# Kernel optimization log

Hardware: AMD Instinct MI355X
Metric: run time of the kernel (lower is better)

## Reference

```python
import jax, jax.numpy as jnp
import numpy as np

D_MODEL = 2048
N_HEADS = 16
HEAD_DIM = D_MODEL // N_HEADS


def setup_inputs() -> dict:
    key = jax.random.key(0)
    k_x, k_wqkv, k_bqkv, k_wo, k_bo = jax.random.split(key, 5)
    s = 1.0 / np.sqrt(D_MODEL)
    return {
        "x": jax.random.normal(k_x, (2, 2048, D_MODEL), dtype=jnp.float32),
        "w_qkv": jax.random.uniform(k_wqkv, (D_MODEL, 3 * D_MODEL), jnp.float32, -s, s),
        "b_qkv": jax.random.uniform(k_bqkv, (3 * D_MODEL,), jnp.float32, -s, s),
        "w_out": jax.random.uniform(k_wo, (D_MODEL, D_MODEL), jnp.float32, -s, s),
        "b_out": jax.random.uniform(k_bo, (D_MODEL,), jnp.float32, -s, s),
    }


def reference(x, w_qkv, b_qkv, w_out, b_out):
    b, l, d = x.shape
    h, e = N_HEADS, HEAD_DIM
    qkv = x @ w_qkv + b_qkv                       # [b, l, 3d]
    q, k, v = jnp.split(qkv, 3, axis=-1)
    # split heads: [b, l, d] -> [b, l, h, e]
    q = q.reshape(b, l, h, e)
    k = k.reshape(b, l, h, e)
    v = v.reshape(b, l, h, e)
    scale = 1.0 / np.sqrt(e).astype(np.float32)
    scores = jnp.einsum("bqhe,bkhe->bhqk", q, k) * scale  # [b, h, l, l]
    attn = jax.nn.softmax(scores, axis=-1)                 # non-causal (module hardcodes is_causal=False)
    out = jnp.einsum("bhqk,bkhe->bqhe", attn, v)           # [b, l, h, e]
    out = out.reshape(b, l, d)                             # merge heads
    return out @ w_out + b_out
```

## Files before the change

### kernel.cpp

```cpp
#include <hip/hip_runtime.h>

typedef __attribute__((ext_vector_type(8))) short bf16x8;
typedef __attribute__((ext_vector_type(4))) float f32x4;
typedef __attribute__((ext_vector_type(16))) float f32x16;
typedef __attribute__((ext_vector_type(4))) int int4v;
typedef __attribute__((ext_vector_type(4))) unsigned short us4;

#define LOG2E 1.4426950408889634f

__device__ __forceinline__ unsigned short f2b(float f){
  unsigned u = __builtin_bit_cast(unsigned, f);
  u = (u + 0x7fffu + ((u >> 16) & 1u)) >> 16;
  return (unsigned short)u;
}
__device__ __forceinline__ unsigned short f2bf(float f){
  unsigned u = __builtin_bit_cast(unsigned, f);
  return (unsigned short)((u + 0x8000u) >> 16);
}

__device__ __forceinline__ f32x4 mfma16(bf16x8 a, bf16x8 b, f32x4 c){
  return __builtin_amdgcn_mfma_f32_16x16x32_bf16(a, b, c, 0, 0, 0);
}
__device__ __forceinline__ f32x16 mfma32(bf16x8 a, bf16x8 b, f32x16 c){
  return __builtin_amdgcn_mfma_f32_32x32x16_bf16(a, b, c, 0, 0, 0);
}

typedef const __attribute__((address_space(1))) void* gas_t;
typedef __attribute__((address_space(3))) void* las_t;
__device__ __forceinline__ void glds16(const void* g, void* l){
  __builtin_amdgcn_global_load_lds((gas_t)g, (las_t)l, 16, 0, 0);
}

__global__ __launch_bounds__(256) void cast_bf16_kernel(const float4* __restrict__ in,
                                                        us4* __restrict__ out, int n4){
  int i = blockIdx.x * 256 + threadIdx.x;
  int stride = gridDim.x * 256;
  for (; i < n4; i += stride){
    float4 v = in[i];
    us4 o; o.x = f2b(v.x); o.y = f2b(v.y); o.z = f2b(v.z); o.w = f2b(v.w);
    out[i] = o;
  }
}

__global__ __launch_bounds__(256) void transpose2_kernel(const float* __restrict__ in0,
                                                         unsigned short* __restrict__ out0,
                                                         const float* __restrict__ in1,
                                                         unsigned short* __restrict__ out1){
  __shared__ float tile[64][65];
  const int tid = threadIdx.x;
  const bool first = blockIdx.x < 96;
  const float* in = first ? in0 : in1;
  unsigned short* out = first ? out0 : out1;
  const int C = first ? 6144 : 2048;
  const int R = 2048;
  const int bx = first ? blockIdx.x : blockIdx.x - 96;
  const int c0 = bx * 64, r0 = blockIdx.y * 64;
#pragma unroll
  for (int p = 0; p < 4; p++){
    int idx = p * 1024 + tid * 4;
    int rr = idx >> 6, cc = idx & 63;
    float4 v = *(const float4*)(in + (size_t)(r0 + rr) * C + (c0 + cc));
    tile[rr][cc+0] = v.x; tile[rr][cc+1] = v.y; tile[rr][cc+2] = v.z; tile[rr][cc+3] = v.w;
  }
  __syncthreads();
#pragma unroll
  for (int p = 0; p < 4; p++){
    int idx = p * 1024 + tid * 4;
    int crow = idx >> 6, rcol = idx & 63;
    us4 o;
    o.x = f2b(tile[rcol+0][crow]); o.y = f2b(tile[rcol+1][crow]);
    o.z = f2b(tile[rcol+2][crow]); o.w = f2b(tile[rcol+3][crow]);
    *(us4*)(out + (size_t)(c0 + crow) * R + (r0 + rcol)) = o;
  }
}

template<int MODE>
__global__ __launch_bounds__(256, 2) void gemm_kernel(
    const unsigned short* __restrict__ A,
    const unsigned short* __restrict__ BT,
    const float* __restrict__ bias,
    unsigned short* __restrict__ qb,
    unsigned short* __restrict__ kb,
    unsigned short* __restrict__ vtb,
    float* __restrict__ outp,
    int cpx, int nbm)
{
  constexpr int K = 2048;
  constexpr int NT = K / 64;
  __shared__ short lA[2][128 * 64];
  __shared__ short lB[2][128 * 64];
  const int tid = threadIdx.x, lane = tid & 63, wid = tid >> 6;
  const int l16 = lane & 15, lhi = lane >> 4;
  const int wr = wid >> 1, wc = wid & 1;

  const int id = blockIdx.x;
  const int logical = (id & 7) * cpx + (id >> 3);
  const int bm = logical % nbm, bn = logical / nbm;

  const char* Abase = (const char*)(A + (size_t)bm * 128 * K);
  const char* Bbase = (const char*)(BT + (size_t)bn * 128 * K);

  const char* agp[4]; const char* bgp[4];
  int dst[4];
#pragma unroll
  for (int i = 0; i < 4; i++){
    int c = wid * 4 + i;
    int row = c * 8 + (lane >> 3);
    int col = ((lane & 7) * 16) ^ ((lane >> 3) << 4);
    agp[i] = Abase + (size_t)row * (K * 2) + col;
    bgp[i] = Bbase + (size_t)row * (K * 2) + col;
    dst[i] = c * 1024;
  }

  auto stage = [&](int kt, int buf){
    char* bA = (char*)lA[buf]; char* bB = (char*)lB[buf];
#pragma unroll
    for (int i = 0; i < 4; i++){
      glds16(agp[i] + kt * 128, bA + dst[i]);
      glds16(bgp[i] + kt * 128, bB + dst[i]);
    }
  };

  f32x4 acc[4][4];
  f32x4 z = {0.f, 0.f, 0.f, 0.f};
#pragma unroll
  for (int i = 0; i < 4; i++)
#pragma unroll
    for (int j = 0; j < 4; j++) acc[i][j] = z;

  stage(0, 0);
  __syncthreads();
  int cur = 0;
  for (int kt = 0; kt < NT; ++kt){
    if (kt + 1 < NT) stage(kt + 1, cur ^ 1);
#pragma unroll
    for (int kk = 0; kk < 2; kk++){
      bf16x8 af[4], bfr[4];
#pragma unroll
      for (int mf = 0; mf < 4; mf++){
        int row = wr * 64 + mf * 16 + l16;
        int byte = (row * 128 + kk * 64 + lhi * 16) ^ ((row & 7) << 4);
        af[mf] = *(const bf16x8*)((const char*)lA[cur] + byte);
      }
#pragma unroll
      for (int nf = 0; nf < 4; nf++){
        int row = wc * 64 + nf * 16 + l16;
        int byte = (row * 128 + kk * 64 + lhi * 16) ^ ((row & 7) << 4);
        bfr[nf] = *(const bf16x8*)((const char*)lB[cur] + byte);
      }
      __builtin_amdgcn_s_setprio(1);
#pragma unroll
      for (int mf = 0; mf < 4; mf++)
#pragma unroll
        for (int nf = 0; nf < 4; nf++)
          acc[mf][nf] = mfma16(af[mf], bfr[nf], acc[mf][nf]);
      __builtin_amdgcn_s_setprio(0);
    }
    __syncthreads();
    cur ^= 1;
  }

  const int row0 = bm * 128 + wr * 64;
  const int col0 = bn * 128 + wc * 64;
  if (MODE == 0){
#pragma unroll
    for (int nf = 0; nf < 4; nf++){
      int colb = col0 + nf * 16;
      float bv = bias[colb + l16];
      int which = colb >> 11;
      int h = (colb >> 7) & 15;
      int e = (colb & 127) + l16;
#pragma unroll
      for (int mf = 0; mf < 4; mf++){
#pragma unroll
        for (int r = 0; r < 4; r++){
          int row = row0 + mf * 16 + lhi * 4 + r;
          int b = row >> 11, t = row & 2047;
          float v = acc[mf][nf][r] + bv;
          size_t bh = (size_t)(b * 16 + h);
          if (which == 0)      qb[(bh * 2048 + t) * 128 + e] = f2b(v * 0.08838834764831845f);
          else if (which == 1) kb[(bh * 2048 + t) * 128 + e] = f2b(v);
          else                 vtb[(bh * 128 + e) * 2048 + t] = f2b(v);
        }
      }
    }
  } else {
#pragma unroll
    for (int nf = 0; nf < 4; nf++){
      int col = col0 + nf * 16 + l16;
      float bv = bias[col];
#pragma unroll
      for (int mf = 0; mf < 4; mf++){
#pragma unroll
        for (int r = 0; r < 4; r++){
          int row = row0 + mf * 16 + lhi * 4 + r;
          outp[(size_t)row * 2048 + col] = acc[mf][nf][r] + bv;
        }
      }
    }
  }
}

__global__ __launch_bounds__(256, 2) void attn_kernel(
    const unsigned short* __restrict__ q_buf,
    const unsigned short* __restrict__ k_buf,
    const unsigned short* __restrict__ vt_buf,
    unsigned short* __restrict__ attn_out)
{
  constexpr int L = 2048, NT = L / 64;
  __shared__ short lK[2][64 * 128];
  __shared__ short lVT[2][128 * 64];
  const int tid = threadIdx.x, lane = tid & 63, wid = tid >> 6;
  const int l31 = lane & 31, lhi2 = lane >> 5;

  const int d = blockIdx.y * 16 + blockIdx.x;
  const int bh = (d & 7) + 8 * ((d >> 3) & 3);
  const int qi = d >> 5;
  const int qbase = qi * 128;

  const unsigned short* qp = q_buf + (size_t)bh * L * 128;
  const char* kp2 = (const char*)(k_buf + (size_t)bh * L * 128);
  const char* vp2 = (const char*)(vt_buf + (size_t)bh * 128 * L);

  bf16x8 qf[8];
  {
    const unsigned short* qr = qp + (size_t)(qbase + wid * 32 + l31) * 128 + lhi2 * 8;
#pragma unroll
    for (int kk = 0; kk < 8; kk++)
      qf[kk] = *(const bf16x8*)(qr + kk * 16);
  }

  const char* kgp[4]; const char* vgp[4];
  int kdst[4], vdst[4];
#pragma unroll
  for (int i = 0; i < 4; i++){
    int c = wid * 4 + i;
    { int row = c * 4 + (lane >> 4);
      int col = ((lane & 15) * 16) ^ ((row & 7) << 4);
      kgp[i] = kp2 + row * 256 + col;
      kdst[i] = c * 1024; }
    { int e = c * 8 + (lane >> 3);
      int col = ((lane & 7) * 16) ^ ((e & 7) << 4);
      vgp[i] = vp2 + (size_t)e * 4096 + col;
      vdst[i] = c * 1024; }
  }

  auto stage = [&](int kt, int buf){
    char* bK = (char*)lK[buf]; char* bV = (char*)lVT[buf];
#pragma unroll
    for (int i = 0; i < 4; i++){
      glds16(kgp[i] + kt * 16384, bK + kdst[i]);
      glds16(vgp[i] + (size_t)kt * 128, bV + vdst[i]);
    }
  };

  f32x16 oacc[4];
#pragma unroll
  for (int nf = 0; nf < 4; nf++)
#pragma unroll
    for (int j = 0; j < 16; j++) oacc[nf][j] = 0.f;
  float m = -1e30f, ml2 = 0.f, lsum = 0.f;

  stage(0, 0);
  __syncthreads();
  int cur = 0;
  for (int kt = 0; kt < NT; ++kt){
    if (kt + 1 < NT) stage(kt + 1, cur ^ 1);
    const char* cK = (const char*)lK[cur];
    const char* cV = (const char*)lVT[cur];

    f32x16 sf[2];
#pragma unroll
    for (int mf = 0; mf < 2; mf++)
#pragma unroll
      for (int j = 0; j < 16; j++) sf[mf][j] = 0.f;
    __builtin_amdgcn_s_setprio(1);
#pragma unroll
    for (int kk = 0; kk < 8; kk++){
#pragma unroll
      for (int mf = 0; mf < 2; mf++){
        int byte = ((l31 * 256 + kk * 32 + lhi2 * 16) ^ ((l31 & 7) << 4)) + mf * 8192;
        bf16x8 kf = *(const bf16x8*)(cK + byte);
        sf[mf] = mfma32(kf, qf[kk], sf[mf]);
      }
    }
    __builtin_amdgcn_s_setprio(0);

    float tm = sf[0][0];
#pragma unroll
    for (int mf = 0; mf < 2; mf++)
#pragma unroll
      for (int j = 0; j < 16; j++) tm = fmaxf(tm, sf[mf][j]);
    tm = fmaxf(tm, __shfl_xor(tm, 32, 64));

    if (!__all(tm <= m + 8.0f)){
      float mn = fmaxf(m, tm);
      float alpha = __builtin_exp2f((m - mn) * LOG2E);
      m = mn; ml2 = mn * LOG2E;
      lsum *= alpha;
#pragma unroll
      for (int reg = 0; reg < 16; reg++){
        int row = (reg & 3) + 8 * (reg >> 2) + 4 * lhi2;
        float ar = __shfl(alpha, row | (lane & 32), 64);
#pragma unroll
        for (int nf = 0; nf < 4; nf++) oacc[nf][reg] *= ar;
      }
    }

    float pex[2][16];
    float rs = 0.f;
#pragma unroll
    for (int mf = 0; mf < 2; mf++)
#pragma unroll
      for (int j = 0; j < 16; j++){
        float p = __builtin_exp2f(__builtin_fmaf(sf[mf][j], LOG2E, -ml2));
        pex[mf][j] = p; rs += p;
      }
    rs += __shfl_xor(rs, 32, 64);
    lsum += rs;

    unsigned W[2][4][2];
#pragma unroll
    for (int mf = 0; mf < 2; mf++)
#pragma unroll
      for (int g = 0; g < 4; g++)
#pragma unroll
        for (int h = 0; h < 2; h++)
          W[mf][g][h] = (unsigned)f2bf(pex[mf][g * 4 + 2 * h]) |
                        ((unsigned)f2bf(pex[mf][g * 4 + 2 * h + 1]) << 16);

    __builtin_amdgcn_s_setprio(1);
#pragma unroll
    for (int kk2 = 0; kk2 < 4; kk2++){
      const int mfp = kk2 >> 1, gA = 2 * (kk2 & 1), gB = gA + 1;
      unsigned A0 = W[mfp][gA][0], A1 = W[mfp][gA][1];
      unsigned B0 = W[mfp][gB][0], B1 = W[mfp][gB][1];
      unsigned own0 = lhi2 ? B0 : A0, own1 = lhi2 ? B1 : A1;
      unsigned snd0 = lhi2 ? A0 : B0, snd1 = lhi2 ? A1 : B1;
      unsigned rcv0 = (unsigned)__shfl_xor((int)snd0, 32, 64);
      unsigned rcv1 = (unsigned)__shfl_xor((int)snd1, 32, 64);
      int4v pw;
      pw.x = (int)(lhi2 ? rcv0 : own0);
      pw.y = (int)(lhi2 ? rcv1 : own1);
      pw.z = (int)(lhi2 ? own0 : rcv0);
      pw.w = (int)(lhi2 ? own1 : rcv1);
      bf16x8 pa = __builtin_bit_cast(bf16x8, pw);
#pragma unroll
      for (int nf = 0; nf < 4; nf++){
        int byte = ((l31 * 128 + kk2 * 32 + lhi2 * 16) ^ ((l31 & 7) << 4)) + nf * 4096;
        bf16x8 vb = *(const bf16x8*)(cV + byte);
        oacc[nf] = mfma32(pa, vb, oacc[nf]);
      }
    }
    __builtin_amdgcn_s_setprio(0);

    __syncthreads();
    cur ^= 1;
  }

  const int b = bh >> 4, h = bh & 15;
  float rl = 1.0f / lsum;
#pragma unroll
  for (int reg = 0; reg < 16; reg++){
    int row = (reg & 3) + 8 * (reg >> 2) + 4 * lhi2;
    float rr = __shfl(rl, row | (lane & 32), 64);
    size_t base = ((size_t)(b * L + qbase + wid * 32 + row)) * 2048 + h * 128 + l31;
#pragma unroll
    for (int nf = 0; nf < 4; nf++)
      attn_out[base + nf * 32] = f2b(oacc[nf][reg] * rr);
  }
}

extern "C" void kernel_launch(void* const* d_in, const int* in_sizes, int n_in,
                              void* d_out, int out_size, void* d_ws, size_t ws_size,
                              hipStream_t stream) {
  const float* x     = (const float*)d_in[0];
  const float* w_qkv = (const float*)d_in[1];
  const float* b_qkv = (const float*)d_in[2];
  const float* w_out = (const float*)d_in[3];
  const float* b_out = (const float*)d_in[4];
  float* out = (float*)d_out;

  unsigned short* ws = (unsigned short*)d_ws;
  unsigned short* xb    = ws;
  unsigned short* wqkvT = xb    + (size_t)4096 * 2048;
  unsigned short* woutT = wqkvT + (size_t)6144 * 2048;
  unsigned short* qb    = woutT + (size_t)2048 * 2048;
  unsigned short* kb    = qb    + (size_t)2 * 16 * 2048 * 128;
  unsigned short* vtb   = kb    + (size_t)2 * 16 * 2048 * 128;
  unsigned short* attnb = vtb   + (size_t)2 * 16 * 2048 * 128;

  cast_bf16_kernel<<<2048, 256, 0, stream>>>((const float4*)x, (us4*)xb, (4096 * 2048) / 4);
  transpose2_kernel<<<dim3(128, 32), 256, 0, stream>>>(w_qkv, wqkvT, w_out, woutT);
  gemm_kernel<0><<<1536, 256, 0, stream>>>(xb, wqkvT, b_qkv, qb, kb, vtb, nullptr, 192, 32);
  attn_kernel<<<dim3(16, 32), 256, 0, stream>>>(qb, kb, vtb, attnb);
  gemm_kernel<1><<<512, 256, 0, stream>>>(attnb, woutT, b_out, nullptr, nullptr, nullptr, out, 64, 32);
}
```

Baseline: 303.4 us.

## Use 512-thread GEMM blocks with 8 waves and drop the block swizzle

The GEMM block grows from 4 to 8 waves, so each wave computes a 64x32 sub-tile instead of 64x64 and global-to-LDS staging is spread over twice as many threads. Fewer accumulators per wave and launch bounds of 4 aim for more resident waves to hide latency. The XCD-aware block index remapping is replaced by a plain 2D grid, which may reduce L2 reuse across chiplets. The 128x128 block tile is unchanged, so each wave does more LDS reads per MFMA.

Result: faster. 276.3 us (-9.0%).

```diff
diff --git a/kernel.cpp b/kernel.cpp
--- a/kernel.cpp
+++ b/kernel.cpp
@@ -75,15 +75,14 @@
 }
 
 template<int MODE>
-__global__ __launch_bounds__(256, 2) void gemm_kernel(
+__global__ __launch_bounds__(512, 4) void gemm_kernel(
     const unsigned short* __restrict__ A,
     const unsigned short* __restrict__ BT,
     const float* __restrict__ bias,
     unsigned short* __restrict__ qb,
     unsigned short* __restrict__ kb,
     unsigned short* __restrict__ vtb,
-    float* __restrict__ outp,
-    int cpx, int nbm)
+    float* __restrict__ outp)
 {
   constexpr int K = 2048;
   constexpr int NT = K / 64;
@@ -91,42 +90,39 @@
   __shared__ short lB[2][128 * 64];
   const int tid = threadIdx.x, lane = tid & 63, wid = tid >> 6;
   const int l16 = lane & 15, lhi = lane >> 4;
-  const int wr = wid >> 1, wc = wid & 1;
-
-  const int id = blockIdx.x;
-  const int logical = (id & 7) * cpx + (id >> 3);
-  const int bm = logical % nbm, bn = logical / nbm;
+  const int wm = wid >> 2, wn = wid & 3;
+  const int bm = blockIdx.x, bn = blockIdx.y;
 
   const char* Abase = (const char*)(A + (size_t)bm * 128 * K);
   const char* Bbase = (const char*)(BT + (size_t)bn * 128 * K);
 
-  const char* agp[4]; const char* bgp[4];
-  int dst[4];
-#pragma unroll
-  for (int i = 0; i < 4; i++){
-    int c = wid * 4 + i;
+  const char* agp[2]; const char* bgp[2];
+  int dst[2];
+#pragma unroll
+  for (int j = 0; j < 2; j++){
+    int c = wid * 2 + j;
     int row = c * 8 + (lane >> 3);
     int col = ((lane & 7) * 16) ^ ((lane >> 3) << 4);
-    agp[i] = Abase + (size_t)row * (K * 2) + col;
-    bgp[i] = Bbase + (size_t)row * (K * 2) + col;
-    dst[i] = c * 1024;
+    agp[j] = Abase + (size_t)row * (K * 2) + col;
+    bgp[j] = Bbase + (size_t)row * (K * 2) + col;
+    dst[j] = c * 1024;
   }
 
   auto stage = [&](int kt, int buf){
     char* bA = (char*)lA[buf]; char* bB = (char*)lB[buf];
 #pragma unroll
-    for (int i = 0; i < 4; i++){
-      glds16(agp[i] + kt * 128, bA + dst[i]);
-      glds16(bgp[i] + kt * 128, bB + dst[i]);
+    for (int j = 0; j < 2; j++){
+      glds16(agp[j] + kt * 128, bA + dst[j]);
+      glds16(bgp[j] + kt * 128, bB + dst[j]);
     }
   };
 
-  f32x4 acc[4][4];
+  f32x4 acc[4][2];
   f32x4 z = {0.f, 0.f, 0.f, 0.f};
 #pragma unroll
   for (int i = 0; i < 4; i++)
 #pragma unroll
-    for (int j = 0; j < 4; j++) acc[i][j] = z;
+    for (int j = 0; j < 2; j++) acc[i][j] = z;
 
   stage(0, 0);
   __syncthreads();
@@ -135,16 +131,16 @@
     if (kt + 1 < NT) stage(kt + 1, cur ^ 1);
 #pragma unroll
     for (int kk = 0; kk < 2; kk++){
-      bf16x8 af[4], bfr[4];
+      bf16x8 af[4], bfr[2];
 #pragma unroll
       for (int mf = 0; mf < 4; mf++){
-        int row = wr * 64 + mf * 16 + l16;
+        int row = wm * 64 + mf * 16 + l16;
         int byte = (row * 128 + kk * 64 + lhi * 16) ^ ((row & 7) << 4);
         af[mf] = *(const bf16x8*)((const char*)lA[cur] + byte);
       }
 #pragma unroll
-      for (int nf = 0; nf < 4; nf++){
-        int row = wc * 64 + nf * 16 + l16;
+      for (int nf = 0; nf < 2; nf++){
+        int row = wn * 32 + nf * 16 + l16;
         int byte = (row * 128 + kk * 64 + lhi * 16) ^ ((row & 7) << 4);
         bfr[nf] = *(const bf16x8*)((const char*)lB[cur] + byte);
       }
@@ -152,7 +148,7 @@
 #pragma unroll
       for (int mf = 0; mf < 4; mf++)
 #pragma unroll
-        for (int nf = 0; nf < 4; nf++)
+        for (int nf = 0; nf < 2; nf++)
           acc[mf][nf] = mfma16(af[mf], bfr[nf], acc[mf][nf]);
       __builtin_amdgcn_s_setprio(0);
     }
@@ -160,11 +156,11 @@
     cur ^= 1;
   }
 
-  const int row0 = bm * 128 + wr * 64;
-  const int col0 = bn * 128 + wc * 64;
+  const int row0 = bm * 128 + wm * 64;
+  const int col0 = bn * 128 + wn * 32;
   if (MODE == 0){
 #pragma unroll
-    for (int nf = 0; nf < 4; nf++){
+    for (int nf = 0; nf < 2; nf++){
       int colb = col0 + nf * 16;
       float bv = bias[colb + l16];
       int which = colb >> 11;
@@ -186,7 +182,7 @@
     }
   } else {
 #pragma unroll
-    for (int nf = 0; nf < 4; nf++){
+    for (int nf = 0; nf < 2; nf++){
       int col = col0 + nf * 16 + l16;
       float bv = bias[col];
 #pragma unroll
@@ -392,7 +388,7 @@
 
   cast_bf16_kernel<<<2048, 256, 0, stream>>>((const float4*)x, (us4*)xb, (4096 * 2048) / 4);
   transpose2_kernel<<<dim3(128, 32), 256, 0, stream>>>(w_qkv, wqkvT, w_out, woutT);
-  gemm_kernel<0><<<1536, 256, 0, stream>>>(xb, wqkvT, b_qkv, qb, kb, vtb, nullptr, 192, 32);
+  gemm_kernel<0><<<dim3(32, 48), 512, 0, stream>>>(xb, wqkvT, b_qkv, qb, kb, vtb, nullptr);
   attn_kernel<<<dim3(16, 32), 256, 0, stream>>>(qb, kb, vtb, attnb);
-  gemm_kernel<1><<<512, 256, 0, stream>>>(attnb, woutT, b_out, nullptr, nullptr, nullptr, out, 64, 32);
-}
+  gemm_kernel<1><<<dim3(32, 16), 512, 0, stream>>>(attnb, woutT, b_out, nullptr, nullptr, nullptr, out);
+}
```
